# Performance work log

Hardware: AMD Instinct MI355X
Metric: run time of the kernel (lower is better)

Reference implementation:

```python
import jax, jax.numpy as jnp
import numpy as np

B, S, HID = 2, 2048, 2048
N_HEADS, HEAD_DIM = 16, 128
SCALE = 1.0 / np.sqrt(HEAD_DIM)
SOFTCAP = 30.0
WINDOW = 1024


def setup_inputs() -> dict:
    key = jax.random.key(0)
    ks = jax.random.split(key, 5)
    w_std = 1.0 / np.sqrt(HID)
    return {
        "x": jax.random.normal(ks[0], (B, S, HID), dtype=jnp.float32),
        "Wq": jax.random.normal(ks[1], (HID, HID), dtype=jnp.float32) * w_std,
        "Wk": jax.random.normal(ks[2], (HID, HID), dtype=jnp.float32) * w_std,
        "Wv": jax.random.normal(ks[3], (HID, HID), dtype=jnp.float32) * w_std,
        "Wo": jax.random.normal(ks[4], (HID, HID), dtype=jnp.float32) * w_std,
    }


def reference(x, Wq, Wk, Wv, Wo):
    b, s, _ = x.shape
    # fused-style QKV projections (nn.Linear: y = x @ W.T), split into heads
    def proj(W):
        y = jnp.einsum('bsh,oh->bso', x, W)
        return y.reshape(b, s, N_HEADS, HEAD_DIM).transpose(0, 2, 1, 3)  # [B,H,S,D]
    q, k, v = proj(Wq), proj(Wk), proj(Wv)

    scores = jnp.einsum('bhsd,bhtd->bhst', q, k) * SCALE  # [B,H,S,S]
    # logit soft-capping: softcap * tanh(logits / softcap)
    scores = SOFTCAP * jnp.tanh(scores / SOFTCAP)

    # causal + sliding-window mask: attend to j in (i - WINDOW, i]
    i = jnp.arange(s)[:, None]
    j = jnp.arange(s)[None, :]
    allowed = (j <= i) & ((i - j) < WINDOW)
    scores = jnp.where(allowed, scores, jnp.finfo(scores.dtype).min)

    p = jax.nn.softmax(scores, axis=-1)
    attn = jnp.einsum('bhst,bhtd->bhsd', p, v)  # [B,H,S,D]
    attn = attn.transpose(0, 2, 1, 3).reshape(b, s, HID)
    out = jnp.einsum('bsh,oh->bso', attn, Wo)
    return out
```

## Files before the change

kernel.cpp:

```cpp
#include <hip/hip_runtime.h>

#define B_SZ 2
#define S_LEN 2048
#define HID_DIM 2048
#define NHEADS 16
#define HEAD_D 128
#define WIN 1024
#define M_ROWS (B_SZ * S_LEN)
#define NXC 8388608

typedef __attribute__((ext_vector_type(8))) short bf16x8;
typedef __attribute__((ext_vector_type(4))) float f32x4;

#define SCALE_F 0.08838834764831845f
#define SOFTCAP_F 30.0f

__device__ __forceinline__ unsigned short f2bf(float f) {
  unsigned u = __builtin_bit_cast(unsigned, f);
  unsigned r = (u + 0x7FFFu + ((u >> 16) & 1u)) >> 16;
  return (unsigned short)r;
}

__device__ __forceinline__ void vmwait6() { asm volatile("s_waitcnt vmcnt(6)" ::: "memory"); }
__device__ __forceinline__ void vmwait0() { asm volatile("s_waitcnt vmcnt(0)" ::: "memory"); }
__device__ __forceinline__ void pbar()    { asm volatile("s_barrier" ::: "memory"); }

__global__ __launch_bounds__(256) void cvt_bf16_kernel(const float* __restrict__ in,
                                                       unsigned short* __restrict__ out,
                                                       int n8, float scale) {
  int i = blockIdx.x * 256 + threadIdx.x;
  if (i >= n8) return;
  const f32x4* p = (const f32x4*)in + (size_t)i * 2;
  f32x4 a = p[0], b = p[1];
  bf16x8 o;
  o[0] = (short)f2bf(a[0] * scale); o[1] = (short)f2bf(a[1] * scale);
  o[2] = (short)f2bf(a[2] * scale); o[3] = (short)f2bf(a[3] * scale);
  o[4] = (short)f2bf(b[0] * scale); o[5] = (short)f2bf(b[1] * scale);
  o[6] = (short)f2bf(b[2] * scale); o[7] = (short)f2bf(b[3] * scale);
  *((bf16x8*)out + i) = o;
}

__device__ __forceinline__ void gload16(const unsigned short* g, unsigned short* l) {
  __builtin_amdgcn_global_load_lds(
      (const __attribute__((address_space(1))) unsigned int*)g,
      (__attribute__((address_space(3))) unsigned int*)l, 16, 0, 0);
}

template <int OMODE>
__global__ __launch_bounds__(512, 2)
void gemm8_kernel(const unsigned short* __restrict__ A,
                  const unsigned short* __restrict__ Bm,
                  void* __restrict__ Out, int nl) {
  extern __shared__ char smem[];
  constexpr int K = 2048, NT = 32;
  constexpr int SLOT = 49152;
  const int t = threadIdx.x;
  const int w = t >> 6, l = t & 63, c = l & 15, g = l >> 4;
  const int wr = w >> 2, wc = w & 3;
  const int xcd = blockIdx.x & 7, q = blockIdx.x >> 3;
  const int mt = q / nl, ntl = q - mt * nl;
  const int nt = xcd * nl + ntl;
  const int m0 = mt * 128, n0 = nt * 256;
  const unsigned short* Ab = A + (size_t)m0 * K;
  const unsigned short* Bb = Bm + (size_t)n0 * K;

  auto lA = [&](int s) { return (unsigned short*)(smem + s * SLOT); };
  auto lB = [&](int s) { return (unsigned short*)(smem + s * SLOT + 16384); };

  auto stA = [&](int tt, int s, int j) {
    int chunk = j * 512 + t, row = chunk >> 3, ch = chunk & 7;
    gload16(Ab + (size_t)row * K + tt * 64 + ((ch ^ (row & 7)) * 8), lA(s) + chunk * 8);
  };
  auto stB = [&](int tt, int s, int j) {
    int chunk = j * 512 + t, row = chunk >> 3, ch = chunk & 7;
    gload16(Bb + (size_t)row * K + tt * 64 + ((ch ^ (row & 7)) * 8), lB(s) + chunk * 8);
  };
  auto rdA = [&](unsigned short* base, int mi, int kk) {
    int row = wr * 64 + mi * 16 + c;
    int ch = (kk * 4 + g) ^ (row & 7);
    return *(const bf16x8*)&base[row * 64 + ch * 8];
  };
  auto rdB = [&](unsigned short* base, int nf, int kk) {
    int row = wc * 64 + nf * 16 + c;
    int ch = (kk * 4 + g) ^ (row & 7);
    return *(const bf16x8*)&base[row * 64 + ch * 8];
  };

  f32x4 acc[4][4];
#pragma unroll
  for (int i = 0; i < 4; ++i)
#pragma unroll
    for (int j = 0; j < 4; ++j) acc[i][j] = (f32x4)0.0f;

  stA(0, 0, 0); stA(0, 0, 1);
  stB(0, 0, 0); stB(0, 0, 1); stB(0, 0, 2); stB(0, 0, 3);
  stA(1, 1, 0); stA(1, 1, 1);
  stB(1, 1, 0); stB(1, 1, 1); stB(1, 1, 2); stB(1, 1, 3);
  vmwait6();
  pbar();

#pragma unroll 1
  for (int tt = 0; tt < NT; ++tt) {
    const int s = tt % 3, ns = (tt + 2) % 3;
    unsigned short* sA = lA(s);
    unsigned short* sB = lB(s);
    const bool pre = (tt + 2) < NT;

    bf16x8 af[4][2], bfr[2][2];
#pragma unroll
    for (int mi = 0; mi < 4; ++mi)
#pragma unroll
      for (int kk = 0; kk < 2; ++kk) af[mi][kk] = rdA(sA, mi, kk);
#pragma unroll
    for (int ni = 0; ni < 2; ++ni)
#pragma unroll
      for (int kk = 0; kk < 2; ++kk) bfr[ni][kk] = rdB(sB, ni, kk);
    if (pre) { stA(tt + 2, ns, 0); stA(tt + 2, ns, 1); stB(tt + 2, ns, 0); }
    pbar();
    __builtin_amdgcn_s_setprio(1);
#pragma unroll
    for (int kk = 0; kk < 2; ++kk)
#pragma unroll
      for (int mi = 0; mi < 4; ++mi)
#pragma unroll
        for (int ni = 0; ni < 2; ++ni)
          acc[mi][ni] = __builtin_amdgcn_mfma_f32_16x16x32_bf16(af[mi][kk], bfr[ni][kk],
                                                                acc[mi][ni], 0, 0, 0);
    __builtin_amdgcn_s_setprio(0);
    pbar();

#pragma unroll
    for (int ni = 0; ni < 2; ++ni)
#pragma unroll
      for (int kk = 0; kk < 2; ++kk) bfr[ni][kk] = rdB(sB, 2 + ni, kk);
    if (pre) { stB(tt + 2, ns, 1); stB(tt + 2, ns, 2); stB(tt + 2, ns, 3); }
    pbar();
    __builtin_amdgcn_s_setprio(1);
#pragma unroll
    for (int kk = 0; kk < 2; ++kk)
#pragma unroll
      for (int mi = 0; mi < 4; ++mi)
#pragma unroll
        for (int ni = 0; ni < 2; ++ni)
          acc[mi][2 + ni] = __builtin_amdgcn_mfma_f32_16x16x32_bf16(af[mi][kk], bfr[ni][kk],
                                                                    acc[mi][2 + ni], 0, 0, 0);
    __builtin_amdgcn_s_setprio(0);
    if (pre) vmwait6(); else vmwait0();
    pbar();
  }

#pragma unroll
  for (int mi = 0; mi < 4; ++mi)
#pragma unroll
    for (int nf = 0; nf < 4; ++nf)
#pragma unroll
      for (int r = 0; r < 4; ++r) {
        int row = m0 + wr * 64 + mi * 16 + g * 4 + r;
        int col = n0 + wc * 64 + nf * 16 + c;
        if (OMODE == 0) {
          int which = col >> 11;
          ((unsigned short*)Out)[(size_t)which * NXC + (size_t)row * 2048 + (col & 2047)] =
              f2bf(acc[mi][nf][r]);
        } else {
          ((float*)Out)[(size_t)row * 2048 + col] = acc[mi][nf][r];
        }
      }
}

__global__ __launch_bounds__(256, 2)
void attn_kernel(const unsigned short* __restrict__ Qb,
                 const unsigned short* __restrict__ Kb,
                 const unsigned short* __restrict__ Vb,
                 unsigned short* __restrict__ Ob) {
  __shared__ unsigned short K_lds[64 * HEAD_D];
  __shared__ unsigned short V_lds[HEAD_D * 64];
  __shared__ unsigned short P_lds[4][32 * 64];

  const int t = threadIdx.x;
  const int w = t >> 6, l = t & 63;
  const int g = l >> 4, c = l & 15;

  const int bid = blockIdx.x;
  const int widx = (bid & 7) * 64 + (bid >> 3);
  const int bh = widx >> 4;
  const int q0 = (widx & 15) * 128;
  const int b = bh >> 4, h = bh & 15;
  const size_t base = (size_t)b * S_LEN * HID_DIM + (size_t)h * HEAD_D;
  const int qw = q0 + w * 32;

  bf16x8 qf[2][4];
#pragma unroll
  for (int qh = 0; qh < 2; ++qh) {
    const unsigned short* qp = Qb + base + (size_t)(qw + qh * 16 + c) * HID_DIM + g * 8;
#pragma unroll
    for (int dch = 0; dch < 4; ++dch) qf[qh][dch] = *(const bf16x8*)(qp + dch * 32);
  }

  f32x4 acc[2][8];
#pragma unroll
  for (int qh = 0; qh < 2; ++qh)
#pragma unroll
    for (int dc = 0; dc < 8; ++dc) acc[qh][dc] = (f32x4)0.0f;
  float lpart[2][4] = {{0, 0, 0, 0}, {0, 0, 0, 0}};

  int kstart = q0 - (WIN - 1);
  if (kstart < 0) kstart = 0;
  kstart &= ~63;
  const int kend = q0 + 127;

  const float C1 = -1.0f / 3.0f, C2 = 2.0f / 15.0f;
  const float CE = SOFTCAP_F * 1.4426950408889634f;

  for (int k0 = kstart; k0 <= kend; k0 += 64) {
#pragma unroll
    for (int i = 0; i < 4; ++i) {
      int li = i * 256 + t;
      int row = li >> 4, chs = li & 15;
      int ch = chs ^ (row & 7);
      gload16(Kb + base + (size_t)(k0 + row) * HID_DIM + ch * 8, &K_lds[li * 8]);
    }
    {
      int m4 = t >> 4, ch = t & 15;
      const unsigned short* vg = Vb + base + (size_t)(k0 + 4 * m4) * HID_DIM + ch * 8;
      bf16x8 v0 = *(const bf16x8*)vg;
      bf16x8 v1 = *(const bf16x8*)(vg + HID_DIM);
      bf16x8 v2 = *(const bf16x8*)(vg + 2 * HID_DIM);
      bf16x8 v3 = *(const bf16x8*)(vg + 3 * HID_DIM);
#pragma unroll
      for (int j = 0; j < 8; ++j) {
        int d = ch * 8 + j;
        int sw = (j ^ ch) & 7;
        int e = (d * 64 + 4 * m4) ^ (sw << 3);
        unsigned long long val =
            (unsigned long long)(unsigned short)v0[j] |
            ((unsigned long long)(unsigned short)v1[j] << 16) |
            ((unsigned long long)(unsigned short)v2[j] << 32) |
            ((unsigned long long)(unsigned short)v3[j] << 48);
        *(unsigned long long*)&V_lds[e] = val;
      }
    }
    __syncthreads();

    if (k0 <= qw + 31 && k0 + 63 >= qw - (WIN - 1)) {
      f32x4 sc[2][4];
#pragma unroll
      for (int qh = 0; qh < 2; ++qh)
#pragma unroll
        for (int kc = 0; kc < 4; ++kc) sc[qh][kc] = (f32x4)0.0f;
#pragma unroll
      for (int kc = 0; kc < 4; ++kc) {
#pragma unroll
        for (int dch = 0; dch < 4; ++dch) {
          int row = kc * 16 + c;
          int e = (row * HEAD_D + dch * 32 + g * 8) ^ ((row & 7) << 3);
          bf16x8 kf = *(const bf16x8*)&K_lds[e];
#pragma unroll
          for (int qh = 0; qh < 2; ++qh)
            sc[qh][kc] = __builtin_amdgcn_mfma_f32_16x16x32_bf16(qf[qh][dch], kf,
                                                                 sc[qh][kc], 0, 0, 0);
        }
      }
#pragma unroll
      for (int qh = 0; qh < 2; ++qh) {
        const int qwh = qw + qh * 16;
        const bool full = (k0 + 63 <= qwh) && (qwh + 15 - k0 < WIN);
#pragma unroll
        for (int kc = 0; kc < 4; ++kc)
#pragma unroll
          for (int r = 0; r < 4; ++r) {
            float y = sc[qh][kc][r];
            float y2 = y * y;
            float tpoly = y * __builtin_fmaf(y2, __builtin_fmaf(y2, C2, C1), 1.0f);
            float pv = __builtin_amdgcn_exp2f(__builtin_fmaf(tpoly, CE, -CE));
            if (!full) {
              int i_g = qwh + g * 4 + r;
              int j_g = k0 + kc * 16 + c;
              bool okm = (j_g <= i_g) && (i_g - j_g < WIN);
              pv = okm ? pv : 0.0f;
            }
            lpart[qh][r] += pv;
            int qq = qh * 16 + g * 4 + r;
            int e = (qq * 64 + kc * 16 + c) ^ ((qq & 7) << 3);
            P_lds[w][e] = f2bf(pv);
          }
      }
      bf16x8 pa[2][2];
#pragma unroll
      for (int qh = 0; qh < 2; ++qh)
#pragma unroll
        for (int kb = 0; kb < 2; ++kb) {
          int row = qh * 16 + c;
          int e = (row * 64 + kb * 32 + g * 8) ^ ((row & 7) << 3);
          pa[qh][kb] = *(const bf16x8*)&P_lds[w][e];
        }
#pragma unroll
      for (int dc = 0; dc < 8; ++dc) {
#pragma unroll
        for (int kb = 0; kb < 2; ++kb) {
          int d = dc * 16 + c;
          int sw = ((d & 7) ^ ((d >> 3) & 7)) & 7;
          int e = (d * 64 + kb * 32 + g * 8) ^ (sw << 3);
          bf16x8 vf = *(const bf16x8*)&V_lds[e];
#pragma unroll
          for (int qh = 0; qh < 2; ++qh)
            acc[qh][dc] = __builtin_amdgcn_mfma_f32_16x16x32_bf16(pa[qh][kb], vf,
                                                                  acc[qh][dc], 0, 0, 0);
        }
      }
    }
    __syncthreads();
  }

#pragma unroll
  for (int qh = 0; qh < 2; ++qh)
#pragma unroll
    for (int r = 0; r < 4; ++r) {
      float rs = lpart[qh][r];
#pragma unroll
      for (int msk = 1; msk < 16; msk <<= 1) rs += __shfl_xor(rs, msk);
      float rinv = 1.0f / rs;
#pragma unroll
      for (int dc = 0; dc < 8; ++dc) {
        int qq = qw + qh * 16 + g * 4 + r;
        float o = acc[qh][dc][r] * rinv;
        Ob[base + (size_t)qq * HID_DIM + dc * 16 + c] = f2bf(o);
      }
    }
}

extern "C" void kernel_launch(void* const* d_in, const int* in_sizes, int n_in,
                              void* d_out, int out_size, void* d_ws, size_t ws_size,
                              hipStream_t stream) {
  const float* x  = (const float*)d_in[0];
  const float* Wq = (const float*)d_in[1];
  const float* Wk = (const float*)d_in[2];
  const float* Wv = (const float*)d_in[3];
  const float* Wo = (const float*)d_in[4];

  const size_t NX = (size_t)M_ROWS * HID_DIM;
  const size_t NW = (size_t)HID_DIM * HID_DIM;

  unsigned short* xb  = (unsigned short*)d_ws;
  unsigned short* Wqb = xb + NX;
  unsigned short* Wkb = Wqb + NW;
  unsigned short* Wvb = Wkb + NW;
  unsigned short* Wob = Wvb + NW;
  unsigned short* Qb  = Wob + NW;
  unsigned short* Kb  = Qb + NX;
  unsigned short* Vb  = Kb + NX;
  unsigned short* Ab  = xb;

  cvt_bf16_kernel<<<dim3((unsigned)(NX / 8 / 256)), 256, 0, stream>>>(x, xb, (int)(NX / 8), 1.0f);
  cvt_bf16_kernel<<<dim3((unsigned)(NW / 8 / 256)), 256, 0, stream>>>(Wq, Wqb, (int)(NW / 8),
                                                                      SCALE_F / SOFTCAP_F);
  cvt_bf16_kernel<<<dim3((unsigned)(NW / 8 / 256)), 256, 0, stream>>>(Wk, Wkb, (int)(NW / 8), 1.0f);
  cvt_bf16_kernel<<<dim3((unsigned)(NW / 8 / 256)), 256, 0, stream>>>(Wv, Wvb, (int)(NW / 8), 1.0f);
  cvt_bf16_kernel<<<dim3((unsigned)(NW / 8 / 256)), 256, 0, stream>>>(Wo, Wob, (int)(NW / 8), 1.0f);

  gemm8_kernel<0><<<dim3(768), 512, 147456, stream>>>(xb, Wqb, Qb, 3);

  attn_kernel<<<dim3(512), 256, 0, stream>>>(Qb, Kb, Vb, Ab);

  gemm8_kernel<1><<<dim3(256), 512, 147456, stream>>>(Ab, Wob, d_out, 1);
}
```

Before: 249.8 us.

## Merge bf16 conversions into one launch and retile QKV GEMM to 256x384

The five fp32-to-bf16 conversion launches become a single kernel that picks its source buffer and scale from the thread index. The QKV projection GEMM is rewritten with larger 256x384 output tiles and a K-step of 32 over a 4-stage ring, with the B loads split across three MFMA phases. This cuts the grid to 256 blocks (one wave on the device) and increases operand reuse per block. The costs are heavier register pressure from 48 accumulators per thread, more LDS per block (160 KB), and more barriers per K-step.

```diff
diff --git a/kernel.cpp b/kernel.cpp
--- a/kernel.cpp
+++ b/kernel.cpp
@@ -21,23 +21,34 @@
   return (unsigned short)r;
 }
 
+__device__ __forceinline__ void vmwait5() { asm volatile("s_waitcnt vmcnt(5)" ::: "memory"); }
 __device__ __forceinline__ void vmwait6() { asm volatile("s_waitcnt vmcnt(6)" ::: "memory"); }
 __device__ __forceinline__ void vmwait0() { asm volatile("s_waitcnt vmcnt(0)" ::: "memory"); }
 __device__ __forceinline__ void pbar()    { asm volatile("s_barrier" ::: "memory"); }
 
-__global__ __launch_bounds__(256) void cvt_bf16_kernel(const float* __restrict__ in,
-                                                       unsigned short* __restrict__ out,
-                                                       int n8, float scale) {
-  int i = blockIdx.x * 256 + threadIdx.x;
-  if (i >= n8) return;
-  const f32x4* p = (const f32x4*)in + (size_t)i * 2;
+__global__ __launch_bounds__(256)
+void cvt_all_kernel(const float* __restrict__ x,  const float* __restrict__ Wq,
+                    const float* __restrict__ Wk, const float* __restrict__ Wv,
+                    const float* __restrict__ Wo, unsigned short* __restrict__ dst) {
+  const int i = blockIdx.x * 256 + threadIdx.x;
+  const int a0 = 1048576;
+  const int aw = 524288;
+  const float* src;
+  float scale = 1.0f;
+  int j = i;
+  if (i < a0) { src = x; }
+  else if (i < a0 + aw)     { src = Wq; j = i - a0;          scale = SCALE_F / SOFTCAP_F; }
+  else if (i < a0 + 2 * aw) { src = Wk; j = i - a0 - aw; }
+  else if (i < a0 + 3 * aw) { src = Wv; j = i - a0 - 2 * aw; }
+  else                      { src = Wo; j = i - a0 - 3 * aw; }
+  const f32x4* p = (const f32x4*)src + (size_t)j * 2;
   f32x4 a = p[0], b = p[1];
   bf16x8 o;
   o[0] = (short)f2bf(a[0] * scale); o[1] = (short)f2bf(a[1] * scale);
   o[2] = (short)f2bf(a[2] * scale); o[3] = (short)f2bf(a[3] * scale);
   o[4] = (short)f2bf(b[0] * scale); o[5] = (short)f2bf(b[1] * scale);
   o[6] = (short)f2bf(b[2] * scale); o[7] = (short)f2bf(b[3] * scale);
-  *((bf16x8*)out + i) = o;
+  *((bf16x8*)dst + i) = o;
 }
 
 __device__ __forceinline__ void gload16(const unsigned short* g, unsigned short* l) {
@@ -46,11 +57,123 @@
       (__attribute__((address_space(3))) unsigned int*)l, 16, 0, 0);
 }
 
-template <int OMODE>
 __global__ __launch_bounds__(512, 2)
-void gemm8_kernel(const unsigned short* __restrict__ A,
-                  const unsigned short* __restrict__ Bm,
-                  void* __restrict__ Out, int nl) {
+void gemm_qkv_kernel(const unsigned short* __restrict__ A,
+                     const unsigned short* __restrict__ Bm,
+                     unsigned short* __restrict__ Out) {
+  extern __shared__ char smem[];
+  constexpr int K = 2048, NT = 64;
+  constexpr int SLOTW = 20480;
+  const int t = threadIdx.x;
+  const int w = t >> 6, l = t & 63, c = l & 15, g = l >> 4;
+  const int wr = w >> 2, wc = w & 3;
+  const int xcd = blockIdx.x & 7, i = blockIdx.x >> 3;
+  const int nt = xcd * 2 + (i & 1), mt = i >> 1;
+  const int m0 = mt * 256, n0 = nt * 384;
+  const unsigned short* Ab = A + (size_t)m0 * K;
+  const unsigned short* Bb = Bm + (size_t)n0 * K;
+
+  int aoff[2], boff[3];
+#pragma unroll
+  for (int j = 0; j < 2; ++j) {
+    int S = j * 512 + t, rp = S >> 3, slu = (S & 7) ^ (rp & 7);
+    aoff[j] = (rp * 2 + (slu >> 2)) * K + (slu & 3) * 8;
+  }
+#pragma unroll
+  for (int j = 0; j < 3; ++j) {
+    int S = j * 512 + t, rp = S >> 3, slu = (S & 7) ^ (rp & 7);
+    boff[j] = (rp * 2 + (slu >> 2)) * K + (slu & 3) * 8;
+  }
+  auto sbase = [&](int s) { return (unsigned short*)smem + s * SLOTW; };
+  auto stA = [&](int tt, int s, int j) {
+    gload16(Ab + aoff[j] + tt * 32, sbase(s) + (j * 512 + t) * 8);
+  };
+  auto stB = [&](int tt, int s, int j) {
+    gload16(Bb + boff[j] + tt * 32, sbase(s) + 8192 + (j * 512 + t) * 8);
+  };
+  auto rix = [&](int row) {
+    return (row >> 1) * 64 + (((((row & 1) << 2) | g) ^ ((row >> 1) & 7)) * 8);
+  };
+
+  f32x4 acc[8][6];
+#pragma unroll
+  for (int mi = 0; mi < 8; ++mi)
+#pragma unroll
+    for (int nf = 0; nf < 6; ++nf) acc[mi][nf] = (f32x4)0.0f;
+
+  stA(0, 0, 0); stA(0, 0, 1); stB(0, 0, 0); stB(0, 0, 1); stB(0, 0, 2);
+  stA(1, 1, 0); stA(1, 1, 1); stB(1, 1, 0); stB(1, 1, 1); stB(1, 1, 2);
+  vmwait5();
+  pbar();
+
+#pragma unroll 1
+  for (int tt = 0; tt < NT; ++tt) {
+    const int s = tt & 3, ns = (tt + 2) & 3;
+    const bool pre = (tt + 2) < NT;
+    unsigned short* sA = sbase(s);
+    unsigned short* sB = sA + 8192;
+
+    bf16x8 af[8], bf[2];
+#pragma unroll
+    for (int mi = 0; mi < 8; ++mi) af[mi] = *(const bf16x8*)&sA[rix(wr * 128 + mi * 16 + c)];
+#pragma unroll
+    for (int nf = 0; nf < 2; ++nf) bf[nf] = *(const bf16x8*)&sB[rix(wc * 96 + nf * 16 + c)];
+    if (pre) { stA(tt + 2, ns, 0); stA(tt + 2, ns, 1); }
+    pbar();
+    __builtin_amdgcn_s_setprio(1);
+#pragma unroll
+    for (int mi = 0; mi < 8; ++mi)
+#pragma unroll
+      for (int nf = 0; nf < 2; ++nf)
+        acc[mi][nf] = __builtin_amdgcn_mfma_f32_16x16x32_bf16(af[mi], bf[nf], acc[mi][nf], 0, 0, 0);
+    __builtin_amdgcn_s_setprio(0);
+    pbar();
+
+#pragma unroll
+    for (int nf = 0; nf < 2; ++nf) bf[nf] = *(const bf16x8*)&sB[rix(wc * 96 + (2 + nf) * 16 + c)];
+    if (pre) { stB(tt + 2, ns, 0); stB(tt + 2, ns, 1); }
+    pbar();
+    __builtin_amdgcn_s_setprio(1);
+#pragma unroll
+    for (int mi = 0; mi < 8; ++mi)
+#pragma unroll
+      for (int nf = 0; nf < 2; ++nf)
+        acc[mi][2 + nf] = __builtin_amdgcn_mfma_f32_16x16x32_bf16(af[mi], bf[nf], acc[mi][2 + nf], 0, 0, 0);
+    __builtin_amdgcn_s_setprio(0);
+    pbar();
+
+#pragma unroll
+    for (int nf = 0; nf < 2; ++nf) bf[nf] = *(const bf16x8*)&sB[rix(wc * 96 + (4 + nf) * 16 + c)];
+    if (pre) { stB(tt + 2, ns, 2); }
+    pbar();
+    __builtin_amdgcn_s_setprio(1);
+#pragma unroll
+    for (int mi = 0; mi < 8; ++mi)
+#pragma unroll
+      for (int nf = 0; nf < 2; ++nf)
+        acc[mi][4 + nf] = __builtin_amdgcn_mfma_f32_16x16x32_bf16(af[mi], bf[nf], acc[mi][4 + nf], 0, 0, 0);
+    __builtin_amdgcn_s_setprio(0);
+    if (pre) vmwait5(); else vmwait0();
+    pbar();
+  }
+
+#pragma unroll
+  for (int mi = 0; mi < 8; ++mi)
+#pragma unroll
+    for (int nf = 0; nf < 6; ++nf)
+#pragma unroll
+      for (int r = 0; r < 4; ++r) {
+        int row = m0 + wr * 128 + mi * 16 + g * 4 + r;
+        int col = n0 + wc * 96 + nf * 16 + c;
+        int which = col >> 11;
+        Out[(size_t)which * NXC + (size_t)row * 2048 + (col & 2047)] = f2bf(acc[mi][nf][r]);
+      }
+}
+
+__global__ __launch_bounds__(512, 2)
+void gemm_wo_kernel(const unsigned short* __restrict__ A,
+                    const unsigned short* __restrict__ Bm,
+                    float* __restrict__ Out) {
   extern __shared__ char smem[];
   constexpr int K = 2048, NT = 32;
   constexpr int SLOT = 49152;
@@ -58,15 +181,13 @@
   const int w = t >> 6, l = t & 63, c = l & 15, g = l >> 4;
   const int wr = w >> 2, wc = w & 3;
   const int xcd = blockIdx.x & 7, q = blockIdx.x >> 3;
-  const int mt = q / nl, ntl = q - mt * nl;
-  const int nt = xcd * nl + ntl;
+  const int mt = q, nt = xcd;
   const int m0 = mt * 128, n0 = nt * 256;
   const unsigned short* Ab = A + (size_t)m0 * K;
   const unsigned short* Bb = Bm + (size_t)n0 * K;
 
   auto lA = [&](int s) { return (unsigned short*)(smem + s * SLOT); };
   auto lB = [&](int s) { return (unsigned short*)(smem + s * SLOT + 16384); };
-
   auto stA = [&](int tt, int s, int j) {
     int chunk = j * 512 + t, row = chunk >> 3, ch = chunk & 7;
     gload16(Ab + (size_t)row * K + tt * 64 + ((ch ^ (row & 7)) * 8), lA(s) + chunk * 8);
@@ -157,13 +278,7 @@
       for (int r = 0; r < 4; ++r) {
         int row = m0 + wr * 64 + mi * 16 + g * 4 + r;
         int col = n0 + wc * 64 + nf * 16 + c;
-        if (OMODE == 0) {
-          int which = col >> 11;
-          ((unsigned short*)Out)[(size_t)which * NXC + (size_t)row * 2048 + (col & 2047)] =
-              f2bf(acc[mi][nf][r]);
-        } else {
-          ((float*)Out)[(size_t)row * 2048 + col] = acc[mi][nf][r];
-        }
+        Out[(size_t)row * 2048 + col] = acc[mi][nf][r];
       }
 }
 
@@ -350,16 +465,11 @@
   unsigned short* Vb  = Kb + NX;
   unsigned short* Ab  = xb;
 
-  cvt_bf16_kernel<<<dim3((unsigned)(NX / 8 / 256)), 256, 0, stream>>>(x, xb, (int)(NX / 8), 1.0f);
-  cvt_bf16_kernel<<<dim3((unsigned)(NW / 8 / 256)), 256, 0, stream>>>(Wq, Wqb, (int)(NW / 8),
-                                                                      SCALE_F / SOFTCAP_F);
-  cvt_bf16_kernel<<<dim3((unsigned)(NW / 8 / 256)), 256, 0, stream>>>(Wk, Wkb, (int)(NW / 8), 1.0f);
-  cvt_bf16_kernel<<<dim3((unsigned)(NW / 8 / 256)), 256, 0, stream>>>(Wv, Wvb, (int)(NW / 8), 1.0f);
-  cvt_bf16_kernel<<<dim3((unsigned)(NW / 8 / 256)), 256, 0, stream>>>(Wo, Wob, (int)(NW / 8), 1.0f);
-
-  gemm8_kernel<0><<<dim3(768), 512, 147456, stream>>>(xb, Wqb, Qb, 3);
+  cvt_all_kernel<<<dim3(12288), 256, 0, stream>>>(x, Wq, Wk, Wv, Wo, xb);
+
+  gemm_qkv_kernel<<<dim3(256), 512, 163840, stream>>>(xb, Wqb, Qb);
 
   attn_kernel<<<dim3(512), 256, 0, stream>>>(Qb, Kb, Vb, Ab);
 
-  gemm8_kernel<1><<<dim3(256), 512, 147456, stream>>>(Ab, Wob, d_out, 1);
-}
+  gemm_wo_kernel<<<dim3(256), 512, 147456, stream>>>(Ab, Wob, (float*)d_out);
+}
```

Result: faster. 223.7 us (-10.5%).
